# Kernel optimization log

Measured on AMD Instinct MI355X. Metric: run time of the kernel, lower is better.

The kernel has to match this reference:

```python
import jax, jax.numpy as jnp
import numpy as np

C = 256
CK = C // 8  # key/query projection channels


def setup_inputs() -> dict:
    key = jax.random.key(0)
    ks = jax.random.split(key, 8)
    B, H, W = 8, 64, 64
    x = jax.random.normal(ks[0], (B, H, W, C), dtype=jnp.float32)
    # 1x1 conv weights are just per-pixel linear maps: [Cin, Cout]
    Wf = jax.random.normal(ks[1], (C, CK), dtype=jnp.float32) * (1.0 / np.sqrt(C))
    bf = jnp.zeros((CK,), dtype=jnp.float32)
    Wg = jax.random.normal(ks[2], (C, CK), dtype=jnp.float32) * (1.0 / np.sqrt(C))
    bg = jnp.zeros((CK,), dtype=jnp.float32)
    Wh = jax.random.normal(ks[3], (C, C), dtype=jnp.float32) * (1.0 / np.sqrt(C))
    bh = jnp.zeros((C,), dtype=jnp.float32)
    gamma = jnp.float32(1.0)
    return {"x": x, "Wf": Wf, "bf": bf, "Wg": Wg, "bg": bg,
            "Wh": Wh, "bh": bh, "gamma": gamma}


def reference(x, Wf, bf, Wg, bg, Wh, bh, gamma):
    B, H, W, Cin = x.shape
    N = H * W
    xf = x.reshape(B, N, Cin)                       # [B, N, C]
    f = xf @ Wf + bf                                 # [B, N, C/8]
    g = xf @ Wg + bg                                 # [B, N, C/8]
    h = xf @ Wh + bh                                 # [B, N, C]
    # s[b,i,j] = <g_i, f_j>  (NOTE: unscaled, g is the "query")
    s = jnp.einsum('bic,bjc->bij', g, f)             # [B, N, N]
    attn = jax.nn.softmax(s, axis=-1)
    out = jnp.einsum('bij,bjc->bic', attn, h)        # [B, N, C]
    out = out.reshape(B, H, W, Cin)
    return gamma * out + x
```

## Files before the change

### kernel.cpp

```cpp
#include <hip/hip_runtime.h>

#define B_ 8
#define NN 4096
#define C_ 256
#define CK_ 32

typedef __attribute__((ext_vector_type(8))) short bf16x8;
typedef __attribute__((ext_vector_type(4))) float f32x4;
typedef __attribute__((ext_vector_type(4))) unsigned int u32x4;

typedef const __attribute__((address_space(1))) void* gas_ptr;
typedef __attribute__((address_space(3))) void* las_ptr;

__device__ __forceinline__ void gload16(const void* src, void* dst) {
    __builtin_amdgcn_global_load_lds((gas_ptr)src, (las_ptr)dst, 16, 0, 0);
}
__device__ __forceinline__ ushort bf16_rne(float v) {
    unsigned u = __builtin_bit_cast(unsigned, v);
    unsigned r = (u + 0x7fffu + ((u >> 16) & 1u)) >> 16;
    return (ushort)r;
}
__device__ __forceinline__ float bf16_to_f(ushort h) {
    return __builtin_bit_cast(float, (unsigned)h << 16);
}
#define MFMA16 __builtin_amdgcn_mfma_f32_16x16x32_bf16

__global__ __launch_bounds__(256) void prep_kernel(
    const float* __restrict__ Wf, const float* __restrict__ Wg,
    const float* __restrict__ Wh,
    ushort* __restrict__ whi, ushort* __restrict__ wlo)
{
    const int idx = blockIdx.x * 256 + threadIdx.x;
    const int e = idx & 7, ll = (idx >> 3) & 63, kc = (idx >> 9) & 7, ct = idx >> 12;
    const int k = kc * 32 + (ll >> 4) * 8 + e;
    const int a = ll & 15;
    float v;
    if (ct < 2)      v = Wf[k * 32 + ct * 16 + a];
    else if (ct < 4) v = Wg[k * 32 + (ct - 2) * 16 + a];
    else             v = Wh[k * 256 + (ct - 4) * 16 + a];
    const ushort hi = bf16_rne(v);
    whi[idx] = hi;
    wlo[idx] = bf16_rne(v - bf16_to_f(hi));
}

__global__ __launch_bounds__(256, 2) void proj_kernel(
    const float* __restrict__ x,
    const ushort* __restrict__ whi, const ushort* __restrict__ wlo,
    const float* __restrict__ bfp, const float* __restrict__ bgp,
    const float* __restrict__ bhp,
    ushort* __restrict__ fh, ushort* __restrict__ fl,
    ushort* __restrict__ gh, ushort* __restrict__ gl,
    ushort* __restrict__ ht)
{
    __shared__ __align__(16) float xs[64 * 256];
    ushort* hs = (ushort*)xs;
    const int tid = threadIdx.x, l = tid & 63, wv = tid >> 6;
    const int g = l >> 4, a = l & 15;
    const int rowbase = blockIdx.x * 64;
    const int bb = rowbase >> 12, n0 = rowbase & 4095;

#pragma unroll
    for (int i = 0; i < 16; i++) {
        const int row = wv * 16 + i;
        const float* src = x + (size_t)(rowbase + row) * 256
                         + ((unsigned)((l * 16) ^ ((i & 7) << 4)) >> 2);
        gload16(src, &xs[row * 256]);
    }
    __syncthreads();

    bf16x8 xh[8], xl[8];
    {
        const int swz = (a & 7) << 4;
        const char* rbase = (const char*)&xs[(wv * 16 + a) * 256];
#pragma unroll
        for (int kc = 0; kc < 8; kc++) {
            f32x4 v0 = *(const f32x4*)(rbase + (((kc * 128 + g * 32) + 0) ^ swz));
            f32x4 v1 = *(const f32x4*)(rbase + (((kc * 128 + g * 32) + 16) ^ swz));
#pragma unroll
            for (int e = 0; e < 4; e++) {
                ushort hi = bf16_rne(v0[e]);
                xh[kc][e] = (short)hi;
                xl[kc][e] = (short)bf16_rne(v0[e] - bf16_to_f(hi));
            }
#pragma unroll
            for (int e = 0; e < 4; e++) {
                ushort hi = bf16_rne(v1[e]);
                xh[kc][4 + e] = (short)hi;
                xl[kc][4 + e] = (short)bf16_rne(v1[e] - bf16_to_f(hi));
            }
        }
    }
    __syncthreads();

#pragma unroll
    for (int ct = 0; ct < 20; ct++) {
        f32x4 acc = (f32x4){0.f, 0.f, 0.f, 0.f};
#pragma unroll
        for (int kc = 0; kc < 8; kc++) {
            const size_t fo = (size_t)((ct * 8 + kc) * 64 + l) * 8;
            bf16x8 wh = *(const bf16x8*)(whi + fo);
            bf16x8 wl = *(const bf16x8*)(wlo + fo);
            if (ct < 4) {
                acc = MFMA16(wh, xh[kc], acc, 0, 0, 0);
                acc = MFMA16(wh, xl[kc], acc, 0, 0, 0);
                acc = MFMA16(wl, xh[kc], acc, 0, 0, 0);
            } else {
                acc = MFMA16(xh[kc], wh, acc, 0, 0, 0);
                acc = MFMA16(xl[kc], wh, acc, 0, 0, 0);
                acc = MFMA16(xh[kc], wl, acc, 0, 0, 0);
            }
        }
        if (ct < 4) {
            const float* bias = (ct < 2) ? bfp : bgp;
            const int colbase = (ct & 1) * 16 + g * 4;
            float4 bv = *(const float4*)&bias[colbase];
            float v0 = acc[0] + bv.x, v1 = acc[1] + bv.y;
            float v2 = acc[2] + bv.z, v3 = acc[3] + bv.w;
            ushort h0 = bf16_rne(v0), h1 = bf16_rne(v1), h2 = bf16_rne(v2), h3 = bf16_rne(v3);
            ushort l0 = bf16_rne(v0 - bf16_to_f(h0)), l1 = bf16_rne(v1 - bf16_to_f(h1));
            ushort l2 = bf16_rne(v2 - bf16_to_f(h2)), l3 = bf16_rne(v3 - bf16_to_f(h3));
            uint2 hw, lw;
            hw.x = (unsigned)h0 | ((unsigned)h1 << 16); hw.y = (unsigned)h2 | ((unsigned)h3 << 16);
            lw.x = (unsigned)l0 | ((unsigned)l1 << 16); lw.y = (unsigned)l2 | ((unsigned)l3 << 16);
            const size_t o = (size_t)(rowbase + wv * 16 + a) * 32 + colbase;
            if (ct < 2) { *(uint2*)&fh[o] = hw; *(uint2*)&fl[o] = lw; }
            else        { *(uint2*)&gh[o] = hw; *(uint2*)&gl[o] = lw; }
        } else {
            const int c = (ct - 4) * 16 + a;
            const float bias = bhp[c];
            ushort h0 = bf16_rne(acc[0] + bias), h1 = bf16_rne(acc[1] + bias);
            ushort h2 = bf16_rne(acc[2] + bias), h3 = bf16_rne(acc[3] + bias);
            uint2 w;
            w.x = (unsigned)h0 | ((unsigned)h1 << 16);
            w.y = (unsigned)h2 | ((unsigned)h3 << 16);
            *(uint2*)&hs[c * 80 + wv * 16 + g * 4] = w;
        }
    }
    __syncthreads();

#pragma unroll
    for (int p = 0; p < 8; p++) {
        const int c = p * 32 + (tid >> 3);
        const int col = (tid & 7) * 8;
        u32x4 v = *(const u32x4*)&hs[c * 80 + col];
        *(u32x4*)&ht[(size_t)(bb * 256 + c) * 4096 + n0 + col] = v;
    }
}

__global__ __launch_bounds__(256, 2) void attn_kernel(
    const ushort* __restrict__ fh, const ushort* __restrict__ fl,
    const ushort* __restrict__ gh, const ushort* __restrict__ gl,
    const ushort* __restrict__ ht, const float* __restrict__ x,
    const float* __restrict__ gammap, float* __restrict__ out)
{
    __shared__ __align__(16) ushort Fh[2][2048];
    __shared__ __align__(16) ushort Fl[2][2048];
    __shared__ __align__(16) ushort Hts[2][16384];

    const int tid = threadIdx.x;
    const int l = tid & 63, wv = tid >> 6;
    const int g = l >> 4, a = l & 15;
    const int bid = blockIdx.x;
    const int swzb = ((bid & 7) << 6) + (bid >> 3);
    const int b = swzb >> 6;
    const int q0 = (swzb & 63) * 64;
    const int base = b * NN;

    const size_t grow = (size_t)(base + q0 + wv * 16 + a) * CK_ + g * 8;
    const bf16x8 agh = *(const bf16x8*)(gh + grow);
    const bf16x8 agl = *(const bf16x8*)(gl + grow);

    float m = -1e30f, lsum = 0.f;
    f32x4 acc[16];
#pragma unroll
    for (int ct = 0; ct < 16; ct++) acc[ct] = (f32x4){0.f, 0.f, 0.f, 0.f};

    auto stage = [&](int buf, int kt) {
        const size_t frow = (size_t)(base + kt * 64 + wv * 16 + a) * CK_ + g * 8;
        gload16(fh + frow, &Fh[buf][wv * 512]);
        gload16(fl + frow, &Fl[buf][wv * 512]);
#pragma unroll
        for (int i = 0; i < 8; i++) {
            const int fr = wv * 8 + i;
            const int khh = fr >> 4, ct = fr & 15;
            const ushort* hsrc = ht + (size_t)(b * 256 + ct * 16 + a) * 4096
                                    + (size_t)(kt * 64 + khh * 32 + g * 8);
            gload16(hsrc, &Hts[buf][fr * 512]);
        }
    };

    stage(0, 0);
    __syncthreads();

    for (int kt = 0; kt < NN / 64; kt++) {
        const int cur = kt & 1;
        if (kt < NN / 64 - 1) stage(cur ^ 1, kt + 1);

        f32x4 s4[4];
#pragma unroll
        for (int s = 0; s < 4; s++) {
            bf16x8 bhk = *(const bf16x8*)&Fh[cur][(s * 64 + l) * 8];
            bf16x8 blk = *(const bf16x8*)&Fl[cur][(s * 64 + l) * 8];
            f32x4 z = (f32x4){0.f, 0.f, 0.f, 0.f};
            z = MFMA16(bhk, agh, z, 0, 0, 0);
            z = MFMA16(blk, agh, z, 0, 0, 0);
            z = MFMA16(bhk, agl, z, 0, 0, 0);
            s4[s] = z;
        }

        float pm = s4[0][0];
#pragma unroll
        for (int s = 0; s < 4; s++)
#pragma unroll
            for (int r = 0; r < 4; r++) pm = fmaxf(pm, s4[s][r]);
        pm = fmaxf(pm, __shfl_xor(pm, 16));
        pm = fmaxf(pm, __shfl_xor(pm, 32));

        const int defer = (pm <= m + 8.f);
        if (!__all(defer)) {
            const float mn = fmaxf(m, pm);
            const float scq = __expf(m - mn);
            m = mn; lsum *= scq;
            float scr[4];
#pragma unroll
            for (int r = 0; r < 4; r++) scr[r] = __shfl(scq, g * 4 + r);
#pragma unroll
            for (int ct = 0; ct < 16; ct++)
#pragma unroll
                for (int r = 0; r < 4; r++) acc[ct][r] *= scr[r];
        }

        float p[4][4], rsum = 0.f;
#pragma unroll
        for (int s = 0; s < 4; s++)
#pragma unroll
            for (int r = 0; r < 4; r++) {
                const float pe = __expf(s4[s][r] - m);
                p[s][r] = pe;
                rsum += pe;
            }
        rsum += __shfl_xor(rsum, 16);
        rsum += __shfl_xor(rsum, 32);
        lsum += rsum;

        unsigned cw[4][2];
#pragma unroll
        for (int s = 0; s < 4; s++) {
            cw[s][0] = (unsigned)bf16_rne(p[s][0]) | ((unsigned)bf16_rne(p[s][1]) << 16);
            cw[s][1] = (unsigned)bf16_rne(p[s][2]) | ((unsigned)bf16_rne(p[s][3]) << 16);
        }

        const int src0 = ((g & 1) << 5) + a;
        const int src1 = src0 + 16;
#pragma unroll
        for (int kh = 0; kh < 2; kh++) {
            const unsigned A0 = (unsigned)__shfl((int)cw[kh * 2][0], src0);
            const unsigned A1 = (unsigned)__shfl((int)cw[kh * 2][1], src0);
            const unsigned A2 = (unsigned)__shfl((int)cw[kh * 2][0], src1);
            const unsigned A3 = (unsigned)__shfl((int)cw[kh * 2][1], src1);
            const unsigned B0 = (unsigned)__shfl((int)cw[kh * 2 + 1][0], src0);
            const unsigned B1 = (unsigned)__shfl((int)cw[kh * 2 + 1][1], src0);
            const unsigned B2 = (unsigned)__shfl((int)cw[kh * 2 + 1][0], src1);
            const unsigned B3 = (unsigned)__shfl((int)cw[kh * 2 + 1][1], src1);
            const int hi = g >> 1;
            u32x4 pw;
            pw[0] = hi ? B0 : A0; pw[1] = hi ? B1 : A1;
            pw[2] = hi ? B2 : A2; pw[3] = hi ? B3 : A3;
            const bf16x8 pa = __builtin_bit_cast(bf16x8, pw);
#pragma unroll
            for (int ct = 0; ct < 16; ct++) {
                bf16x8 hb = *(const bf16x8*)&Hts[cur][((kh * 16 + ct) * 64 + l) * 8];
                acc[ct] = MFMA16(pa, hb, acc[ct], 0, 0, 0);
            }
        }

        __syncthreads();
    }

    const float gamma = *gammap;
    const float inv = 1.f / lsum;
    float invr[4];
#pragma unroll
    for (int r = 0; r < 4; r++) invr[r] = __shfl(inv, g * 4 + r);
#pragma unroll
    for (int ct = 0; ct < 16; ct++) {
#pragma unroll
        for (int r = 0; r < 4; r++) {
            const int row = base + q0 + wv * 16 + g * 4 + r;
            const int o = row * C_ + ct * 16 + a;
            out[o] = fmaf(gamma, acc[ct][r] * invr[r], x[o]);
        }
    }
}

extern "C" void kernel_launch(void* const* d_in, const int* in_sizes, int n_in,
                              void* d_out, int out_size, void* d_ws, size_t ws_size,
                              hipStream_t stream) {
    const float* x     = (const float*)d_in[0];
    const float* Wf    = (const float*)d_in[1];
    const float* bfp   = (const float*)d_in[2];
    const float* Wg    = (const float*)d_in[3];
    const float* bgp   = (const float*)d_in[4];
    const float* Wh    = (const float*)d_in[5];
    const float* bhp   = (const float*)d_in[6];
    const float* gamma = (const float*)d_in[7];
    float* out = (float*)d_out;

    const size_t npix = (size_t)B_ * NN;
    ushort* fh  = (ushort*)d_ws;
    ushort* fl  = fh + npix * CK_;
    ushort* gh  = fl + npix * CK_;
    ushort* gl  = gh + npix * CK_;
    ushort* ht  = gl + npix * CK_;
    ushort* whi = ht + (size_t)B_ * C_ * NN;
    ushort* wlo = whi + 20 * 8 * 64 * 8;

    prep_kernel<<<320, 256, 0, stream>>>(Wf, Wg, Wh, whi, wlo);
    proj_kernel<<<(B_ * NN) / 64, 256, 0, stream>>>(x, whi, wlo, bfp, bgp, bhp,
                                                    fh, fl, gh, gl, ht);
    attn_kernel<<<B_ * (NN / 64), 256, 0, stream>>>(fh, fl, gh, gl, ht, x, gamma, out);
}
```

Before: 293.4 us.

## Double query rows per attention wave and split projection columns across waves

The attention kernel now gives each wave 32 query rows instead of 16, using two accumulator sets. This halves the number of blocks and halves the global-to-LDS traffic for F and H tiles per query, since each staged K/V tile is reused for twice as many queries. The price is roughly double the register use, with launch bounds lowered to one block per SIMD, which reduces occupancy and latency hiding. The projection kernel now stores x as pre-split bf16 hi/lo in shared memory and gives each wave 5 output column tiles across all 64 rows, instead of each wave computing all 20 tiles for its own 16 rows, which cuts the redundant weight loads per wave.

```diff
diff --git a/kernel.cpp b/kernel.cpp
--- a/kernel.cpp
+++ b/kernel.cpp
@@ -52,88 +52,113 @@
     ushort* __restrict__ gh, ushort* __restrict__ gl,
     ushort* __restrict__ ht)
 {
-    __shared__ __align__(16) float xs[64 * 256];
-    ushort* hs = (ushort*)xs;
+    __shared__ __align__(16) ushort sbuf[32768];
     const int tid = threadIdx.x, l = tid & 63, wv = tid >> 6;
     const int g = l >> 4, a = l & 15;
     const int rowbase = blockIdx.x * 64;
     const int bb = rowbase >> 12, n0 = rowbase & 4095;
 
-#pragma unroll
-    for (int i = 0; i < 16; i++) {
-        const int row = wv * 16 + i;
-        const float* src = x + (size_t)(rowbase + row) * 256
-                         + ((unsigned)((l * 16) ^ ((i & 7) << 4)) >> 2);
-        gload16(src, &xs[row * 256]);
+    {
+        const int r = tid >> 2, cq = tid & 3;
+        const float* xrow = x + (size_t)(rowbase + r) * 256;
+        const unsigned swz = (unsigned)((r & 7) << 4);
+#pragma unroll
+        for (int j = 0; j < 16; j++) {
+            float4 v = *(const float4*)&xrow[cq * 4 + j * 16];
+            ushort h0 = bf16_rne(v.x), h1 = bf16_rne(v.y);
+            ushort h2 = bf16_rne(v.z), h3 = bf16_rne(v.w);
+            uint2 hw, lw;
+            hw.x = (unsigned)h0 | ((unsigned)h1 << 16);
+            hw.y = (unsigned)h2 | ((unsigned)h3 << 16);
+            lw.x = (unsigned)bf16_rne(v.x - bf16_to_f(h0)) |
+                   ((unsigned)bf16_rne(v.y - bf16_to_f(h1)) << 16);
+            lw.y = (unsigned)bf16_rne(v.z - bf16_to_f(h2)) |
+                   ((unsigned)bf16_rne(v.w - bf16_to_f(h3)) << 16);
+            const unsigned byt = (unsigned)(r * 512 + cq * 8 + j * 32) ^ swz;
+            *(uint2*)&sbuf[byt >> 1] = hw;
+            *(uint2*)&sbuf[16384 + (byt >> 1)] = lw;
+        }
     }
     __syncthreads();
 
-    bf16x8 xh[8], xl[8];
-    {
-        const int swz = (a & 7) << 4;
-        const char* rbase = (const char*)&xs[(wv * 16 + a) * 256];
-#pragma unroll
-        for (int kc = 0; kc < 8; kc++) {
-            f32x4 v0 = *(const f32x4*)(rbase + (((kc * 128 + g * 32) + 0) ^ swz));
-            f32x4 v1 = *(const f32x4*)(rbase + (((kc * 128 + g * 32) + 16) ^ swz));
-#pragma unroll
-            for (int e = 0; e < 4; e++) {
-                ushort hi = bf16_rne(v0[e]);
-                xh[kc][e] = (short)hi;
-                xl[kc][e] = (short)bf16_rne(v0[e] - bf16_to_f(hi));
-            }
-#pragma unroll
-            for (int e = 0; e < 4; e++) {
-                ushort hi = bf16_rne(v1[e]);
-                xh[kc][4 + e] = (short)hi;
-                xl[kc][4 + e] = (short)bf16_rne(v1[e] - bf16_to_f(hi));
-            }
-        }
-    }
-    __syncthreads();
-
-#pragma unroll
-    for (int ct = 0; ct < 20; ct++) {
-        f32x4 acc = (f32x4){0.f, 0.f, 0.f, 0.f};
+    f32x4 acc[5][4];
+#pragma unroll
+    for (int ci = 0; ci < 5; ci++)
+#pragma unroll
+        for (int rg = 0; rg < 4; rg++) acc[ci][rg] = (f32x4){0.f, 0.f, 0.f, 0.f};
+
+#pragma unroll
+    for (int ci = 0; ci < 5; ci++) {
+        const int ct = wv * 5 + ci;
 #pragma unroll
         for (int kc = 0; kc < 8; kc++) {
             const size_t fo = (size_t)((ct * 8 + kc) * 64 + l) * 8;
-            bf16x8 wh = *(const bf16x8*)(whi + fo);
-            bf16x8 wl = *(const bf16x8*)(wlo + fo);
-            if (ct < 4) {
-                acc = MFMA16(wh, xh[kc], acc, 0, 0, 0);
-                acc = MFMA16(wh, xl[kc], acc, 0, 0, 0);
-                acc = MFMA16(wl, xh[kc], acc, 0, 0, 0);
-            } else {
-                acc = MFMA16(xh[kc], wh, acc, 0, 0, 0);
-                acc = MFMA16(xl[kc], wh, acc, 0, 0, 0);
-                acc = MFMA16(xh[kc], wl, acc, 0, 0, 0);
-            }
-        }
+            const bf16x8 wh = *(const bf16x8*)(whi + fo);
+            const bf16x8 wl = *(const bf16x8*)(wlo + fo);
+#pragma unroll
+            for (int rg = 0; rg < 4; rg++) {
+                const unsigned byt = (unsigned)((rg * 16 + a) * 512 + kc * 64 + g * 16)
+                                     ^ (unsigned)((a & 7) << 4);
+                const bf16x8 xhf = *(const bf16x8*)&sbuf[byt >> 1];
+                const bf16x8 xlf = *(const bf16x8*)&sbuf[16384 + (byt >> 1)];
+                if (ct < 4) {
+                    acc[ci][rg] = MFMA16(wh, xhf, acc[ci][rg], 0, 0, 0);
+                    acc[ci][rg] = MFMA16(wh, xlf, acc[ci][rg], 0, 0, 0);
+                    acc[ci][rg] = MFMA16(wl, xhf, acc[ci][rg], 0, 0, 0);
+                } else {
+                    acc[ci][rg] = MFMA16(xhf, wh, acc[ci][rg], 0, 0, 0);
+                    acc[ci][rg] = MFMA16(xlf, wh, acc[ci][rg], 0, 0, 0);
+                    acc[ci][rg] = MFMA16(xhf, wl, acc[ci][rg], 0, 0, 0);
+                }
+            }
+        }
+    }
+
+#pragma unroll
+    for (int ci = 0; ci < 5; ci++) {
+        const int ct = wv * 5 + ci;
         if (ct < 4) {
             const float* bias = (ct < 2) ? bfp : bgp;
             const int colbase = (ct & 1) * 16 + g * 4;
             float4 bv = *(const float4*)&bias[colbase];
-            float v0 = acc[0] + bv.x, v1 = acc[1] + bv.y;
-            float v2 = acc[2] + bv.z, v3 = acc[3] + bv.w;
-            ushort h0 = bf16_rne(v0), h1 = bf16_rne(v1), h2 = bf16_rne(v2), h3 = bf16_rne(v3);
-            ushort l0 = bf16_rne(v0 - bf16_to_f(h0)), l1 = bf16_rne(v1 - bf16_to_f(h1));
-            ushort l2 = bf16_rne(v2 - bf16_to_f(h2)), l3 = bf16_rne(v3 - bf16_to_f(h3));
-            uint2 hw, lw;
-            hw.x = (unsigned)h0 | ((unsigned)h1 << 16); hw.y = (unsigned)h2 | ((unsigned)h3 << 16);
-            lw.x = (unsigned)l0 | ((unsigned)l1 << 16); lw.y = (unsigned)l2 | ((unsigned)l3 << 16);
-            const size_t o = (size_t)(rowbase + wv * 16 + a) * 32 + colbase;
-            if (ct < 2) { *(uint2*)&fh[o] = hw; *(uint2*)&fl[o] = lw; }
-            else        { *(uint2*)&gh[o] = hw; *(uint2*)&gl[o] = lw; }
-        } else {
+#pragma unroll
+            for (int rg = 0; rg < 4; rg++) {
+                float v0 = acc[ci][rg][0] + bv.x, v1 = acc[ci][rg][1] + bv.y;
+                float v2 = acc[ci][rg][2] + bv.z, v3 = acc[ci][rg][3] + bv.w;
+                ushort h0 = bf16_rne(v0), h1 = bf16_rne(v1);
+                ushort h2 = bf16_rne(v2), h3 = bf16_rne(v3);
+                uint2 hw, lw;
+                hw.x = (unsigned)h0 | ((unsigned)h1 << 16);
+                hw.y = (unsigned)h2 | ((unsigned)h3 << 16);
+                lw.x = (unsigned)bf16_rne(v0 - bf16_to_f(h0)) |
+                       ((unsigned)bf16_rne(v1 - bf16_to_f(h1)) << 16);
+                lw.y = (unsigned)bf16_rne(v2 - bf16_to_f(h2)) |
+                       ((unsigned)bf16_rne(v3 - bf16_to_f(h3)) << 16);
+                const size_t o = (size_t)(rowbase + rg * 16 + a) * 32 + colbase;
+                if (ct < 2) { *(uint2*)&fh[o] = hw; *(uint2*)&fl[o] = lw; }
+                else        { *(uint2*)&gh[o] = hw; *(uint2*)&gl[o] = lw; }
+            }
+        }
+    }
+    __syncthreads();
+
+#pragma unroll
+    for (int ci = 0; ci < 5; ci++) {
+        const int ct = wv * 5 + ci;
+        if (ct >= 4) {
             const int c = (ct - 4) * 16 + a;
             const float bias = bhp[c];
-            ushort h0 = bf16_rne(acc[0] + bias), h1 = bf16_rne(acc[1] + bias);
-            ushort h2 = bf16_rne(acc[2] + bias), h3 = bf16_rne(acc[3] + bias);
-            uint2 w;
-            w.x = (unsigned)h0 | ((unsigned)h1 << 16);
-            w.y = (unsigned)h2 | ((unsigned)h3 << 16);
-            *(uint2*)&hs[c * 80 + wv * 16 + g * 4] = w;
+#pragma unroll
+            for (int rg = 0; rg < 4; rg++) {
+                ushort h0 = bf16_rne(acc[ci][rg][0] + bias);
+                ushort h1 = bf16_rne(acc[ci][rg][1] + bias);
+                ushort h2 = bf16_rne(acc[ci][rg][2] + bias);
+                ushort h3 = bf16_rne(acc[ci][rg][3] + bias);
+                uint2 w;
+                w.x = (unsigned)h0 | ((unsigned)h1 << 16);
+                w.y = (unsigned)h2 | ((unsigned)h3 << 16);
+                *(uint2*)&sbuf[c * 80 + rg * 16 + g * 4] = w;
+            }
         }
     }
     __syncthreads();
@@ -142,12 +167,12 @@
     for (int p = 0; p < 8; p++) {
         const int c = p * 32 + (tid >> 3);
         const int col = (tid & 7) * 8;
-        u32x4 v = *(const u32x4*)&hs[c * 80 + col];
+        u32x4 v = *(const u32x4*)&sbuf[c * 80 + col];
         *(u32x4*)&ht[(size_t)(bb * 256 + c) * 4096 + n0 + col] = v;
     }
 }
 
-__global__ __launch_bounds__(256, 2) void attn_kernel(
+__global__ __launch_bounds__(256, 1) void attn_kernel(
     const ushort* __restrict__ fh, const ushort* __restrict__ fl,
     const ushort* __restrict__ gh, const ushort* __restrict__ gl,
     const ushort* __restrict__ ht, const float* __restrict__ x,
@@ -161,19 +186,24 @@
     const int l = tid & 63, wv = tid >> 6;
     const int g = l >> 4, a = l & 15;
     const int bid = blockIdx.x;
-    const int swzb = ((bid & 7) << 6) + (bid >> 3);
-    const int b = swzb >> 6;
-    const int q0 = (swzb & 63) * 64;
+    const int swzb = ((bid & 7) << 5) + (bid >> 3);
+    const int b = swzb >> 5;
+    const int q0 = (swzb & 31) * 128;
     const int base = b * NN;
 
-    const size_t grow = (size_t)(base + q0 + wv * 16 + a) * CK_ + g * 8;
-    const bf16x8 agh = *(const bf16x8*)(gh + grow);
-    const bf16x8 agl = *(const bf16x8*)(gl + grow);
-
-    float m = -1e30f, lsum = 0.f;
-    f32x4 acc[16];
-#pragma unroll
-    for (int ct = 0; ct < 16; ct++) acc[ct] = (f32x4){0.f, 0.f, 0.f, 0.f};
+    const size_t grow0 = (size_t)(base + q0 + wv * 32 + a) * CK_ + g * 8;
+    const bf16x8 agh0 = *(const bf16x8*)(gh + grow0);
+    const bf16x8 agl0 = *(const bf16x8*)(gl + grow0);
+    const bf16x8 agh1 = *(const bf16x8*)(gh + grow0 + 16 * CK_);
+    const bf16x8 agl1 = *(const bf16x8*)(gl + grow0 + 16 * CK_);
+
+    float m0 = -1e30f, ls0 = 0.f, m1 = -1e30f, ls1 = 0.f;
+    f32x4 acc0[16], acc1[16];
+#pragma unroll
+    for (int ct = 0; ct < 16; ct++) {
+        acc0[ct] = (f32x4){0.f, 0.f, 0.f, 0.f};
+        acc1[ct] = (f32x4){0.f, 0.f, 0.f, 0.f};
+    }
 
     auto stage = [&](int buf, int kt) {
         const size_t frow = (size_t)(base + kt * 64 + wv * 16 + a) * CK_ + g * 8;
@@ -196,81 +226,108 @@
         const int cur = kt & 1;
         if (kt < NN / 64 - 1) stage(cur ^ 1, kt + 1);
 
-        f32x4 s4[4];
+        f32x4 s40[4], s41[4];
 #pragma unroll
         for (int s = 0; s < 4; s++) {
-            bf16x8 bhk = *(const bf16x8*)&Fh[cur][(s * 64 + l) * 8];
-            bf16x8 blk = *(const bf16x8*)&Fl[cur][(s * 64 + l) * 8];
-            f32x4 z = (f32x4){0.f, 0.f, 0.f, 0.f};
-            z = MFMA16(bhk, agh, z, 0, 0, 0);
-            z = MFMA16(blk, agh, z, 0, 0, 0);
-            z = MFMA16(bhk, agl, z, 0, 0, 0);
-            s4[s] = z;
-        }
-
-        float pm = s4[0][0];
+            const bf16x8 bhk = *(const bf16x8*)&Fh[cur][(s * 64 + l) * 8];
+            const bf16x8 blk = *(const bf16x8*)&Fl[cur][(s * 64 + l) * 8];
+            f32x4 z0 = (f32x4){0.f, 0.f, 0.f, 0.f};
+            z0 = MFMA16(bhk, agh0, z0, 0, 0, 0);
+            z0 = MFMA16(blk, agh0, z0, 0, 0, 0);
+            z0 = MFMA16(bhk, agl0, z0, 0, 0, 0);
+            s40[s] = z0;
+            f32x4 z1 = (f32x4){0.f, 0.f, 0.f, 0.f};
+            z1 = MFMA16(bhk, agh1, z1, 0, 0, 0);
+            z1 = MFMA16(blk, agh1, z1, 0, 0, 0);
+            z1 = MFMA16(bhk, agl1, z1, 0, 0, 0);
+            s41[s] = z1;
+        }
+
+        float pm0 = s40[0][0], pm1 = s41[0][0];
 #pragma unroll
         for (int s = 0; s < 4; s++)
 #pragma unroll
-            for (int r = 0; r < 4; r++) pm = fmaxf(pm, s4[s][r]);
-        pm = fmaxf(pm, __shfl_xor(pm, 16));
-        pm = fmaxf(pm, __shfl_xor(pm, 32));
-
-        const int defer = (pm <= m + 8.f);
+            for (int r = 0; r < 4; r++) {
+                pm0 = fmaxf(pm0, s40[s][r]);
+                pm1 = fmaxf(pm1, s41[s][r]);
+            }
+        pm0 = fmaxf(pm0, __shfl_xor(pm0, 16)); pm0 = fmaxf(pm0, __shfl_xor(pm0, 32));
+        pm1 = fmaxf(pm1, __shfl_xor(pm1, 16)); pm1 = fmaxf(pm1, __shfl_xor(pm1, 32));
+
+        const int defer = (pm0 <= m0 + 8.f) && (pm1 <= m1 + 8.f);
         if (!__all(defer)) {
-            const float mn = fmaxf(m, pm);
-            const float scq = __expf(m - mn);
-            m = mn; lsum *= scq;
-            float scr[4];
-#pragma unroll
-            for (int r = 0; r < 4; r++) scr[r] = __shfl(scq, g * 4 + r);
+            const float mn0 = fmaxf(m0, pm0), mn1 = fmaxf(m1, pm1);
+            const float sc0 = __expf(m0 - mn0), sc1 = __expf(m1 - mn1);
+            m0 = mn0; ls0 *= sc0; m1 = mn1; ls1 *= sc1;
+            float scr0[4], scr1[4];
+#pragma unroll
+            for (int r = 0; r < 4; r++) {
+                scr0[r] = __shfl(sc0, g * 4 + r);
+                scr1[r] = __shfl(sc1, g * 4 + r);
+            }
 #pragma unroll
             for (int ct = 0; ct < 16; ct++)
 #pragma unroll
-                for (int r = 0; r < 4; r++) acc[ct][r] *= scr[r];
-        }
-
-        float p[4][4], rsum = 0.f;
-#pragma unroll
-        for (int s = 0; s < 4; s++)
-#pragma unroll
-            for (int r = 0; r < 4; r++) {
-                const float pe = __expf(s4[s][r] - m);
-                p[s][r] = pe;
-                rsum += pe;
-            }
-        rsum += __shfl_xor(rsum, 16);
-        rsum += __shfl_xor(rsum, 32);
-        lsum += rsum;
-
-        unsigned cw[4][2];
+                for (int r = 0; r < 4; r++) {
+                    acc0[ct][r] *= scr0[r];
+                    acc1[ct][r] *= scr1[r];
+                }
+        }
+
+        float rs0 = 0.f, rs1 = 0.f;
+        unsigned cw0[4][2], cw1[4][2];
 #pragma unroll
         for (int s = 0; s < 4; s++) {
-            cw[s][0] = (unsigned)bf16_rne(p[s][0]) | ((unsigned)bf16_rne(p[s][1]) << 16);
-            cw[s][1] = (unsigned)bf16_rne(p[s][2]) | ((unsigned)bf16_rne(p[s][3]) << 16);
-        }
+            float a0 = __expf(s40[s][0] - m0), a1 = __expf(s40[s][1] - m0);
+            float a2 = __expf(s40[s][2] - m0), a3 = __expf(s40[s][3] - m0);
+            rs0 += (a0 + a1) + (a2 + a3);
+            cw0[s][0] = (unsigned)bf16_rne(a0) | ((unsigned)bf16_rne(a1) << 16);
+            cw0[s][1] = (unsigned)bf16_rne(a2) | ((unsigned)bf16_rne(a3) << 16);
+            float b0 = __expf(s41[s][0] - m1), b1 = __expf(s41[s][1] - m1);
+            float b2 = __expf(s41[s][2] - m1), b3 = __expf(s41[s][3] - m1);
+            rs1 += (b0 + b1) + (b2 + b3);
+            cw1[s][0] = (unsigned)bf16_rne(b0) | ((unsigned)bf16_rne(b1) << 16);
+            cw1[s][1] = (unsigned)bf16_rne(b2) | ((unsigned)bf16_rne(b3) << 16);
+        }
+        rs0 += __shfl_xor(rs0, 16); rs0 += __shfl_xor(rs0, 32); ls0 += rs0;
+        rs1 += __shfl_xor(rs1, 16); rs1 += __shfl_xor(rs1, 32); ls1 += rs1;
 
         const int src0 = ((g & 1) << 5) + a;
         const int src1 = src0 + 16;
+        const int hi = g >> 1;
 #pragma unroll
         for (int kh = 0; kh < 2; kh++) {
-            const unsigned A0 = (unsigned)__shfl((int)cw[kh * 2][0], src0);
-            const unsigned A1 = (unsigned)__shfl((int)cw[kh * 2][1], src0);
-            const unsigned A2 = (unsigned)__shfl((int)cw[kh * 2][0], src1);
-            const unsigned A3 = (unsigned)__shfl((int)cw[kh * 2][1], src1);
-            const unsigned B0 = (unsigned)__shfl((int)cw[kh * 2 + 1][0], src0);
-            const unsigned B1 = (unsigned)__shfl((int)cw[kh * 2 + 1][1], src0);
-            const unsigned B2 = (unsigned)__shfl((int)cw[kh * 2 + 1][0], src1);
-            const unsigned B3 = (unsigned)__shfl((int)cw[kh * 2 + 1][1], src1);
-            const int hi = g >> 1;
-            u32x4 pw;
-            pw[0] = hi ? B0 : A0; pw[1] = hi ? B1 : A1;
-            pw[2] = hi ? B2 : A2; pw[3] = hi ? B3 : A3;
-            const bf16x8 pa = __builtin_bit_cast(bf16x8, pw);
+            const unsigned A0 = (unsigned)__shfl((int)cw0[kh * 2][0], src0);
+            const unsigned A1 = (unsigned)__shfl((int)cw0[kh * 2][1], src0);
+            const unsigned A2 = (unsigned)__shfl((int)cw0[kh * 2][0], src1);
+            const unsigned A3 = (unsigned)__shfl((int)cw0[kh * 2][1], src1);
+            const unsigned B0 = (unsigned)__shfl((int)cw0[kh * 2 + 1][0], src0);
+            const unsigned B1 = (unsigned)__shfl((int)cw0[kh * 2 + 1][1], src0);
+            const unsigned B2 = (unsigned)__shfl((int)cw0[kh * 2 + 1][0], src1);
+            const unsigned B3 = (unsigned)__shfl((int)cw0[kh * 2 + 1][1], src1);
+            u32x4 pw0;
+            pw0[0] = hi ? B0 : A0; pw0[1] = hi ? B1 : A1;
+            pw0[2] = hi ? B2 : A2; pw0[3] = hi ? B3 : A3;
+            const bf16x8 pa0 = __builtin_bit_cast(bf16x8, pw0);
+
+            const unsigned C0 = (unsigned)__shfl((int)cw1[kh * 2][0], src0);
+            const unsigned C1 = (unsigned)__shfl((int)cw1[kh * 2][1], src0);
+            const unsigned C2 = (unsigned)__shfl((int)cw1[kh * 2][0], src1);
+            const unsigned C3 = (unsigned)__shfl((int)cw1[kh * 2][1], src1);
+            const unsigned D0 = (unsigned)__shfl((int)cw1[kh * 2 + 1][0], src0);
+            const unsigned D1 = (unsigned)__shfl((int)cw1[kh * 2 + 1][1], src0);
+            const unsigned D2 = (unsigned)__shfl((int)cw1[kh * 2 + 1][0], src1);
+            const unsigned D3 = (unsigned)__shfl((int)cw1[kh * 2 + 1][1], src1);
+            u32x4 pw1;
+            pw1[0] = hi ? D0 : C0; pw1[1] = hi ? D1 : C1;
+            pw1[2] = hi ? D2 : C2; pw1[3] = hi ? D3 : C3;
+            const bf16x8 pa1 = __builtin_bit_cast(bf16x8, pw1);
+
 #pragma unroll
             for (int ct = 0; ct < 16; ct++) {
-                bf16x8 hb = *(const bf16x8*)&Hts[cur][((kh * 16 + ct) * 64 + l) * 8];
-                acc[ct] = MFMA16(pa, hb, acc[ct], 0, 0, 0);
+                const bf16x8 hb = *(const bf16x8*)&Hts[cur][((kh * 16 + ct) * 64 + l) * 8];
+                acc0[ct] = MFMA16(pa0, hb, acc0[ct], 0, 0, 0);
+                acc1[ct] = MFMA16(pa1, hb, acc1[ct], 0, 0, 0);
             }
         }
 
@@ -278,17 +335,22 @@
     }
 
     const float gamma = *gammap;
-    const float inv = 1.f / lsum;
-    float invr[4];
-#pragma unroll
-    for (int r = 0; r < 4; r++) invr[r] = __shfl(inv, g * 4 + r);
+    const float inv0 = 1.f / ls0, inv1 = 1.f / ls1;
+    float invr0[4], invr1[4];
+#pragma unroll
+    for (int r = 0; r < 4; r++) {
+        invr0[r] = __shfl(inv0, g * 4 + r);
+        invr1[r] = __shfl(inv1, g * 4 + r);
+    }
 #pragma unroll
     for (int ct = 0; ct < 16; ct++) {
 #pragma unroll
         for (int r = 0; r < 4; r++) {
-            const int row = base + q0 + wv * 16 + g * 4 + r;
-            const int o = row * C_ + ct * 16 + a;
-            out[o] = fmaf(gamma, acc[ct][r] * invr[r], x[o]);
+            const int row0 = base + q0 + wv * 32 + g * 4 + r;
+            const int o0 = row0 * C_ + ct * 16 + a;
+            out[o0] = fmaf(gamma, acc0[ct][r] * invr0[r], x[o0]);
+            const int o1 = o0 + 16 * C_;
+            out[o1] = fmaf(gamma, acc1[ct][r] * invr1[r], x[o1]);
         }
     }
 }
@@ -318,5 +380,5 @@
     prep_kernel<<<320, 256, 0, stream>>>(Wf, Wg, Wh, whi, wlo);
     proj_kernel<<<(B_ * NN) / 64, 256, 0, stream>>>(x, whi, wlo, bfp, bgp, bhp,
                                                     fh, fl, gh, gl, ht);
-    attn_kernel<<<B_ * (NN / 64), 256, 0, stream>>>(fh, fl, gh, gl, ht, x, gamma, out);
-}
+    attn_kernel<<<B_ * (NN / 128), 256, 0, stream>>>(fh, fl, gh, gl, ht, x, gamma, out);
+}
```

After: 361.2 us. 23.1% more time.
